# Kernel optimization log

Hardware: AMD Instinct MI355X
Metric: run time of the kernel (lower is better)

The kernel has to match this reference:

```python
import jax, jax.numpy as jnp
import numpy as np

N_PTS = 1 << 20          # query points
N_LEVELS = 8
BASE_RES, MAX_RES = 16, 512
GROWTH = (MAX_RES / BASE_RES) ** (1.0 / (N_LEVELS - 1))
RES = [int(np.floor(BASE_RES * GROWTH ** i)) for i in range(N_LEVELS)]
T = 1 << 19              # hash table size per level
F = 2                    # features per table entry
D = 64                   # per-level MLP width
NUM_OUT = 16
BOUND = 1.5

# 8 corner offsets of a unit cube, and NGP spatial-hash primes
OFFSETS = np.stack(np.meshgrid(*([[0, 1]] * 3), indexing='ij'), -1).reshape(8, 3)
PRIMES = np.array([1, 2654435761, 805459861], dtype=np.uint32)


def hash_interp(xn, table, res):
    """Trilinear hash-grid lookup. xn: [N,3] in [0,1), table: [T,F]."""
    pos = xn * res                                    # [N,3]
    p0f = jnp.floor(pos)
    w = pos - jax.lax.stop_gradient(p0f)              # [N,3] interp weights
    p0 = jax.lax.stop_gradient(p0f).astype(jnp.uint32)
    corners = p0[:, None, :] + jnp.asarray(OFFSETS.astype(np.uint32))[None]  # [N,8,3]
    hp = corners * jnp.asarray(PRIMES)[None, None, :]  # uint32 wraparound mul
    idx = (hp[..., 0] ^ hp[..., 1] ^ hp[..., 2]) & jnp.uint32(T - 1)  # [N,8]
    feats = table[idx]                                # [N,8,F] irregular gather
    off = jnp.asarray(OFFSETS.astype(np.float32))     # [8,3]
    wc = jnp.prod(off[None] * w[:, None, :] + (1.0 - off[None]) * (1.0 - w[:, None, :]), axis=-1)  # [N,8]
    return jnp.einsum('nc,ncf->nf', wc, feats)        # [N,F]


def fourier(h, B):
    """Fourier feature embed: h [N,D] @ B [N_freqs] -> [sin, cos]."""
    proj = (2.0 * jnp.pi) * (h @ B)                   # [N, D//2]
    return jnp.concatenate([jnp.sin(proj), jnp.cos(proj)], axis=-1)  # [N, D]


def setup_inputs() -> dict:
    key = jax.random.key(0)
    ks = jax.random.split(key, 12)
    inp = {
        'input': jax.random.normal(ks[0], (N_PTS, 3), jnp.float32),
        'W0': jax.random.normal(ks[1], (3, D), jnp.float32) * 0.3,
        'b0': jnp.zeros((D,), jnp.float32),
        'Ws': jax.random.normal(ks[2], (N_LEVELS - 1, D, D), jnp.float32) * (1.0 / np.sqrt(D)),
        'bs': jnp.zeros((N_LEVELS - 1, D), jnp.float32),
        'tables': jax.random.uniform(ks[3], (N_LEVELS, T, F), jnp.float32, -1e-2, 1e-2),
        'Gw': jax.random.normal(ks[4], (N_LEVELS, F, D), jnp.float32) * 0.5,
        'Gb': jnp.zeros((N_LEVELS, D), jnp.float32),
        'Bmat': jax.random.normal(ks[5], (N_LEVELS, D, D // 2), jnp.float32) * 0.25,
        'Wout': jax.random.normal(ks[6], (D, NUM_OUT), jnp.float32) * (1.0 / np.sqrt(D)),
        'bout': jnp.zeros((NUM_OUT,), jnp.float32),
    }
    return inp


def reference(input, W0, b0, Ws, bs, tables, Gw, Gb, Bmat, Wout, bout):
    x = input / BOUND                                  # [N,3]
    xn = jnp.clip((x + 1.0) * 0.5, 0.0, 1.0 - 1e-6)    # normalize to [0,1)
    h = x
    acc = jnp.zeros((input.shape[0], D), jnp.float32)
    for i in range(N_LEVELS):
        h = (h @ W0 + b0) if i == 0 else (h @ Ws[i - 1] + bs[i - 1])  # [N,D]
        g = hash_interp(xn, tables[i], float(RES[i]))  # [N,F] hash-grid feats
        hg = h + g @ Gw[i] + Gb[i]                     # fuse grid feats into channel
        acc = acc + fourier(hg, Bmat[i])               # [N,D] sin/cos embed, summed
    return acc @ Wout + bout                           # [N,NUM_OUT]
```

## Files before the change

### kernel.cpp

```cpp
#include <hip/hip_runtime.h>
#include <math.h>
#include <stdint.h>

#define N_LEVELS 8
#define TBITS 19
#define TMASK ((1u << TBITS) - 1u)
#define BLK 128

typedef __attribute__((ext_vector_type(8))) short short8;
typedef __attribute__((ext_vector_type(4))) float f32x4;
typedef unsigned int uint;
typedef unsigned short ushort;

#define WSW_OFF   0
#define WSW_N     (7 * 2 * 4 * 2 * 512)
#define WSB_OFF   (WSW_N * 2)
#define WSB_N     (8 * 2 * 2 * 2 * 512)
#define WSWO_OFF  (WSB_OFF + WSB_N * 2)
#define WSWO_N    (2 * 2 * 512)
#define WSP_OFF   (WSWO_OFF + WSWO_N * 2)
#define WSP_N     (8 * 3 * 32)
#define WS_NEEDED ((size_t)(WSP_OFF + WSP_N * 4))

struct ResArr { float r[N_LEVELS]; };

#define HIDX(pt, ch) ((((pt) << 6) | (ch)) ^ (((pt) & 7) << 3))
#define HLO 2048

__device__ __forceinline__ ushort f2bf(float f) {
    uint u = __float_as_uint(f);
    u += 0x7fffu + ((u >> 16) & 1u);
    return (ushort)(u >> 16);
}
__device__ __forceinline__ float bf2f(ushort h) {
    return __uint_as_float(((uint)h) << 16);
}
__device__ __forceinline__ uint cvtpk(float a, float b) {
    uint r;
    asm("v_cvt_pk_bf16_f32 %0, %1, %2" : "=v"(r) : "v"(a), "v"(b));
    return r;
}
__device__ __forceinline__ short8 ldfragG(const void* p) {
    return __builtin_bit_cast(short8, *(const uint4*)p);
}
__device__ __forceinline__ short8 ldfragL(const ushort* p) {
    return __builtin_bit_cast(short8, *(const uint4*)p);
}
__device__ __forceinline__ f32x4 MFMA(short8 a, short8 b, f32x4 c) {
    return __builtin_amdgcn_mfma_f32_16x16x32_bf16(a, b, c, 0, 0, 0);
}
__device__ __forceinline__ f32x4 zero4() {
    f32x4 z; z[0] = 0.f; z[1] = 0.f; z[2] = 0.f; z[3] = 0.f; return z;
}
__device__ __forceinline__ float sin2pi(float t) {
    return __builtin_amdgcn_sinf(__builtin_amdgcn_fractf(t));
}
__device__ __forceinline__ float cos2pi(float t) {
    return __builtin_amdgcn_cosf(__builtin_amdgcn_fractf(t));
}

__global__ void prep_kernel(const float* __restrict__ Ws,
                            const float* __restrict__ Bmat,
                            const float* __restrict__ Wout,
                            const float* __restrict__ Gw,
                            const float* __restrict__ Gb,
                            void* __restrict__ ws)
{
    const int NW = WSW_N, NB = WSB_N, NWO = WSWO_N;
    const int NTOT = NW + NB + NWO + WSP_N;
    int t = blockIdx.x * 256 + threadIdx.x;
    if (t >= NTOT) return;
    ushort* w16 = (ushort*)ws;
    float* wsP = (float*)((char*)ws + WSP_OFF);

    if (t < NW) {
        int i = t & 7, lane = (t >> 3) & 63, ks = (t >> 9) & 1;
        int mb = (t >> 10) & 3, s = (t >> 12) & 1, lv = t >> 13;
        int gl = lane >> 4, il = lane & 15;
        int k = ks * 32 + gl * 8 + i, m = mb * 16 + il;
        float v = Ws[lv * 4096 + k * 64 + m];
        ushort hi = f2bf(v);
        w16[t] = s ? f2bf(v - bf2f(hi)) : hi;
    } else if (t < NW + NB) {
        int u = t - NW;
        int i = u & 7, lane = (u >> 3) & 63, ks = (u >> 9) & 1;
        int mb = (u >> 10) & 1, s = (u >> 11) & 1, lv = u >> 12;
        int gl = lane >> 4, il = lane & 15;
        int k = ks * 32 + gl * 8 + i, m = mb * 16 + il;
        float v = Bmat[lv * 2048 + k * 32 + m];
        ushort hi = f2bf(v);
        w16[NW + u] = s ? f2bf(v - bf2f(hi)) : hi;
    } else if (t < NW + NB + NWO) {
        int u = t - NW - NB;
        int i = u & 7, lane = (u >> 3) & 63, ks = (u >> 9) & 1, s = (u >> 10) & 1;
        int gl = lane >> 4, il = lane & 15;
        int k = ks * 32 + gl * 8 + i;
        float v = Wout[k * 16 + il];
        ushort hi = f2bf(v);
        w16[(WSWO_OFF / 2) + u] = s ? f2bf(v - bf2f(hi)) : hi;
    } else {
        int u = t - NW - NB - NWO;
        int lv = u / 96, rem = u % 96, wh = rem >> 5, m = rem & 31;
        const float* src = (wh == 0) ? (Gw + lv * 128)
                         : (wh == 1) ? (Gw + lv * 128 + 64)
                                     : (Gb + lv * 64);
        float acc = 0.f;
        for (int j = 0; j < 64; ++j)
            acc = fmaf(src[j], Bmat[lv * 2048 + j * 32 + m], acc);
        wsP[lv * 96 + wh * 32 + m] = acc;
    }
}

__global__ __launch_bounds__(64) void ffb_mfma(
    const float* __restrict__ input,
    const float* __restrict__ W0,
    const float* __restrict__ b0,
    const float* __restrict__ bs,
    const float* __restrict__ tables,
    const float* __restrict__ bout,
    const void* __restrict__ ws,
    float* __restrict__ out,
    int npts, ResArr ra)
{
    __shared__ __attribute__((aligned(16))) ushort sH[4096];
    __shared__ float sP[96];
    __shared__ float sBias[64];
    __shared__ float sG[64];

    const int l = threadIdx.x;
    const int il = l & 15, gl = l >> 4;
    const int base = blockIdx.x * 32;
    const int p = l & 31;
    const char* wsc = (const char*)ws;
    const float* wsP = (const float*)(wsc + WSP_OFF);

    float x0 = input[(size_t)(base + p) * 3 + 0] * (1.0f / 1.5f);
    float x1 = input[(size_t)(base + p) * 3 + 1] * (1.0f / 1.5f);
    float x2 = input[(size_t)(base + p) * 3 + 2] * (1.0f / 1.5f);
    const float hiclip = (float)(1.0 - 1e-6);
    float xn0 = fminf(fmaxf((x0 + 1.0f) * 0.5f, 0.0f), hiclip);
    float xn1 = fminf(fmaxf((x1 + 1.0f) * 0.5f, 0.0f), hiclip);
    float xn2 = fminf(fmaxf((x2 + 1.0f) * 0.5f, 0.0f), hiclip);

    short8 aWo[2];
#pragma unroll
    for (int ks = 0; ks < 2; ++ks)
        aWo[ks] = ldfragG(wsc + WSWO_OFF + (size_t)ks * 1024 + l * 16);

    f32x4 outacc[2];
    outacc[0] = zero4(); outacc[1] = zero4();
    short8 bH0[2][2], bH1[2][2];

    for (int lev = 0; lev < N_LEVELS; ++lev) {
        if (lev > 0) sBias[l] = bs[(lev - 1) * 64 + l];
        sP[l] = wsP[lev * 96 + l];
        if (l < 32) sP[64 + l] = wsP[lev * 96 + 64 + l];
        if (l < 32) {
            const float res = ra.r[lev];
            float px = xn0 * res, py = xn1 * res, pz = xn2 * res;
            float fx = floorf(px), fy = floorf(py), fz = floorf(pz);
            float wx = px - fx, wy = py - fy, wz = pz - fz;
            uint ix = (uint)fx, iy = (uint)fy, iz = (uint)fz;
            const float* __restrict__ tab = tables + (((size_t)lev) << TBITS) * 2;
            float g0 = 0.f, g1 = 0.f;
#pragma unroll
            for (int c = 0; c < 8; ++c) {
                const uint bx = (c >> 2) & 1, by = (c >> 1) & 1, bz = c & 1;
                uint hx = ix + bx;
                uint hy = (iy + by) * 2654435761u;
                uint hz = (iz + bz) * 805459861u;
                uint idx = (hx ^ hy ^ hz) & TMASK;
                float f0 = tab[(size_t)idx * 2 + 0];
                float f1 = tab[(size_t)idx * 2 + 1];
                float wc = (bx ? wx : 1.0f - wx) * (by ? wy : 1.0f - wy) * (bz ? wz : 1.0f - wz);
                g0 = fmaf(wc, f0, g0);
                g1 = fmaf(wc, f1, g1);
            }
            sG[2 * l] = g0; sG[2 * l + 1] = g1;
        }
        __syncthreads();

        if (lev == 0) {
            const int chb = (l >> 5) * 32;
#pragma unroll
            for (int cc = 0; cc < 32; cc += 2) {
                int ch = chb + cc;
                float v0 = fmaf(x0, W0[ch],     fmaf(x1, W0[64 + ch],     fmaf(x2, W0[128 + ch],     b0[ch])));
                float v1 = fmaf(x0, W0[ch + 1], fmaf(x1, W0[64 + ch + 1], fmaf(x2, W0[128 + ch + 1], b0[ch + 1])));
                uint pk = cvtpk(v0, v1);
                float r0 = v0 - __uint_as_float(pk << 16);
                float r1 = v1 - __uint_as_float(pk & 0xffff0000u);
                uint pklo = cvtpk(r0, r1);
                uint idx = HIDX(p, ch);
                *(uint*)&sH[idx] = pk;
                *(uint*)&sH[HLO + idx] = pklo;
            }
        } else {
            f32x4 acc[4][2];
#pragma unroll
            for (int mb = 0; mb < 4; ++mb)
#pragma unroll
                for (int nb = 0; nb < 2; ++nb) acc[mb][nb] = zero4();
#pragma unroll
            for (int mb = 0; mb < 4; ++mb) {
                short8 aHi[2], aLo[2];
#pragma unroll
                for (int ks = 0; ks < 2; ++ks) {
                    aHi[ks] = ldfragG(wsc + WSW_OFF + (size_t)((((lev - 1) * 2 + 0) * 4 + mb) * 2 + ks) * 1024 + l * 16);
                    aLo[ks] = ldfragG(wsc + WSW_OFF + (size_t)((((lev - 1) * 2 + 1) * 4 + mb) * 2 + ks) * 1024 + l * 16);
                }
#pragma unroll
                for (int nb = 0; nb < 2; ++nb)
#pragma unroll
                    for (int ks = 0; ks < 2; ++ks) {
                        acc[mb][nb] = MFMA(aHi[ks], bH0[ks][nb], acc[mb][nb]);
                        acc[mb][nb] = MFMA(aLo[ks], bH0[ks][nb], acc[mb][nb]);
                        acc[mb][nb] = MFMA(aHi[ks], bH1[ks][nb], acc[mb][nb]);
                    }
            }
#pragma unroll
            for (int mb = 0; mb < 4; ++mb)
#pragma unroll
                for (int nb = 0; nb < 2; ++nb) {
                    int pt = nb * 16 + il, ch0 = mb * 16 + gl * 4;
                    float2 ba = *(float2*)&sBias[ch0];
                    float2 bb = *(float2*)&sBias[ch0 + 2];
                    float v0 = acc[mb][nb][0] + ba.x, v1 = acc[mb][nb][1] + ba.y;
                    float v2 = acc[mb][nb][2] + bb.x, v3 = acc[mb][nb][3] + bb.y;
                    uint pkA = cvtpk(v0, v1), pkB = cvtpk(v2, v3);
                    float r0 = v0 - __uint_as_float(pkA << 16);
                    float r1 = v1 - __uint_as_float(pkA & 0xffff0000u);
                    float r2 = v2 - __uint_as_float(pkB << 16);
                    float r3 = v3 - __uint_as_float(pkB & 0xffff0000u);
                    uint pkLA = cvtpk(r0, r1), pkLB = cvtpk(r2, r3);
                    uint idx = HIDX(pt, ch0);
                    *(uint*)&sH[idx] = pkA;        *(uint*)&sH[idx + 2] = pkB;
                    *(uint*)&sH[HLO + idx] = pkLA; *(uint*)&sH[HLO + idx + 2] = pkLB;
                }
        }
        __syncthreads();

#pragma unroll
        for (int ks = 0; ks < 2; ++ks)
#pragma unroll
            for (int nb = 0; nb < 2; ++nb) {
                int pt = nb * 16 + il;
                uint idx = HIDX(pt, ks * 32 + gl * 8);
                bH0[ks][nb] = ldfragL(&sH[idx]);
                bH1[ks][nb] = ldfragL(&sH[HLO + idx]);
            }

        f32x4 pacc[2][2];
#pragma unroll
        for (int mb = 0; mb < 2; ++mb)
#pragma unroll
            for (int nb = 0; nb < 2; ++nb) pacc[mb][nb] = zero4();
#pragma unroll
        for (int mb = 0; mb < 2; ++mb) {
            short8 aBhi[2], aBlo[2];
#pragma unroll
            for (int ks = 0; ks < 2; ++ks) {
                aBhi[ks] = ldfragG(wsc + WSB_OFF + (size_t)(((lev * 2 + 0) * 2 + mb) * 2 + ks) * 1024 + l * 16);
                aBlo[ks] = ldfragG(wsc + WSB_OFF + (size_t)(((lev * 2 + 1) * 2 + mb) * 2 + ks) * 1024 + l * 16);
            }
#pragma unroll
            for (int nb = 0; nb < 2; ++nb)
#pragma unroll
                for (int ks = 0; ks < 2; ++ks) {
                    pacc[mb][nb] = MFMA(aBhi[ks], bH0[ks][nb], pacc[mb][nb]);
                    pacc[mb][nb] = MFMA(aBlo[ks], bH0[ks][nb], pacc[mb][nb]);
                    pacc[mb][nb] = MFMA(aBhi[ks], bH1[ks][nb], pacc[mb][nb]);
                }
        }

#pragma unroll
        for (int mb = 0; mb < 2; ++mb)
#pragma unroll
            for (int nb = 0; nb < 2; ++nb) {
                int pt = nb * 16 + il, m0 = mb * 16 + gl * 4;
                float2 g   = *(float2*)&sG[pt * 2];
                float2 p0a = *(float2*)&sP[m0],      p0b = *(float2*)&sP[m0 + 2];
                float2 p1a = *(float2*)&sP[32 + m0], p1b = *(float2*)&sP[32 + m0 + 2];
                float2 p2a = *(float2*)&sP[64 + m0], p2b = *(float2*)&sP[64 + m0 + 2];
                float t0 = pacc[mb][nb][0] + fmaf(g.x, p0a.x, fmaf(g.y, p1a.x, p2a.x));
                float t1 = pacc[mb][nb][1] + fmaf(g.x, p0a.y, fmaf(g.y, p1a.y, p2a.y));
                float t2 = pacc[mb][nb][2] + fmaf(g.x, p0b.x, fmaf(g.y, p1b.x, p2b.x));
                float t3 = pacc[mb][nb][3] + fmaf(g.x, p0b.y, fmaf(g.y, p1b.y, p2b.y));
                float s0 = sin2pi(t0), s1 = sin2pi(t1), s2 = sin2pi(t2), s3 = sin2pi(t3);
                float c0 = cos2pi(t0), c1 = cos2pi(t1), c2 = cos2pi(t2), c3 = cos2pi(t3);
                uint idxs = HIDX(pt, m0), idxc = HIDX(pt, 32 + m0);
                *(uint*)&sH[HLO + idxs]     = cvtpk(s0, s1);
                *(uint*)&sH[HLO + idxs + 2] = cvtpk(s2, s3);
                *(uint*)&sH[HLO + idxc]     = cvtpk(c0, c1);
                *(uint*)&sH[HLO + idxc + 2] = cvtpk(c2, c3);
            }
        __syncthreads();

#pragma unroll
        for (int nb = 0; nb < 2; ++nb)
#pragma unroll
            for (int ks = 0; ks < 2; ++ks) {
                int pt = nb * 16 + il;
                short8 bF = ldfragL(&sH[HLO + HIDX(pt, ks * 32 + gl * 8)]);
                outacc[nb] = MFMA(aWo[ks], bF, outacc[nb]);
            }
    }

    float4 bo = *(const float4*)&bout[gl * 4];
#pragma unroll
    for (int nb = 0; nb < 2; ++nb) {
        int pt = nb * 16 + il;
        float4 v;
        v.x = outacc[nb][0] + bo.x;
        v.y = outacc[nb][1] + bo.y;
        v.z = outacc[nb][2] + bo.z;
        v.w = outacc[nb][3] + bo.w;
        *(float4*)(&out[(size_t)(base + pt) * 16 + gl * 4]) = v;
    }
}

__global__ __launch_bounds__(BLK) void ffb_valu(
    const float* __restrict__ input,
    const float* __restrict__ W0,
    const float* __restrict__ b0,
    const float* __restrict__ Ws,
    const float* __restrict__ bs,
    const float* __restrict__ tables,
    const float* __restrict__ Gw,
    const float* __restrict__ Gb,
    const float* __restrict__ Bmat,
    const float* __restrict__ Wout,
    const float* __restrict__ bout,
    float* __restrict__ out,
    int npts, ResArr resarr)
{
    __shared__ float lds_h[64][BLK];

    const int tid = threadIdx.x;
    const int n = blockIdx.x * BLK + tid;
    if (n >= npts) return;

    float x0 = input[(size_t)n * 3 + 0] / 1.5f;
    float x1 = input[(size_t)n * 3 + 1] / 1.5f;
    float x2 = input[(size_t)n * 3 + 2] / 1.5f;
    const float hi = (float)(1.0 - 1e-6);
    float xn0 = fminf(fmaxf((x0 + 1.0f) * 0.5f, 0.0f), hi);
    float xn1 = fminf(fmaxf((x1 + 1.0f) * 0.5f, 0.0f), hi);
    float xn2 = fminf(fmaxf((x2 + 1.0f) * 0.5f, 0.0f), hi);

    float outacc[16];
#pragma unroll
    for (int o = 0; o < 16; ++o) outacc[o] = 0.0f;

    for (int lev = 0; lev < N_LEVELS; ++lev) {
        float nh[64];
        if (lev == 0) {
#pragma unroll
            for (int j = 0; j < 64; ++j)
                nh[j] = fmaf(x0, W0[j], fmaf(x1, W0[64 + j], fmaf(x2, W0[128 + j], b0[j])));
        } else {
            const float* __restrict__ Wl = Ws + (size_t)(lev - 1) * 4096;
            const float* __restrict__ bl = bs + (size_t)(lev - 1) * 64;
#pragma unroll
            for (int j = 0; j < 64; ++j) nh[j] = bl[j];
            for (int k = 0; k < 64; ++k) {
                float hk = lds_h[k][tid];
                const float* __restrict__ wrow = Wl + (size_t)k * 64;
#pragma unroll
                for (int j = 0; j < 64; ++j)
                    nh[j] = fmaf(hk, wrow[j], nh[j]);
            }
        }
#pragma unroll
        for (int j = 0; j < 64; ++j) lds_h[j][tid] = nh[j];

        const float res = resarr.r[lev];
        float px = xn0 * res, py = xn1 * res, pz = xn2 * res;
        float fx = floorf(px), fy = floorf(py), fz = floorf(pz);
        float wx = px - fx, wy = py - fy, wz = pz - fz;
        uint32_t ix = (uint32_t)fx, iy = (uint32_t)fy, iz = (uint32_t)fz;
        const float* __restrict__ tab = tables + ((size_t)lev << TBITS) * 2;
        float g0 = 0.0f, g1 = 0.0f;
#pragma unroll
        for (int c = 0; c < 8; ++c) {
            const uint32_t bx = (c >> 2) & 1, by = (c >> 1) & 1, bz = c & 1;
            uint32_t hx = (ix + bx);
            uint32_t hy = (iy + by) * 2654435761u;
            uint32_t hz = (iz + bz) * 805459861u;
            uint32_t idx = (hx ^ hy ^ hz) & TMASK;
            float f0 = tab[(size_t)idx * 2 + 0];
            float f1 = tab[(size_t)idx * 2 + 1];
            float wc = (bx ? wx : 1.0f - wx) * (by ? wy : 1.0f - wy) * (bz ? wz : 1.0f - wz);
            g0 = fmaf(wc, f0, g0);
            g1 = fmaf(wc, f1, g1);
        }

        const float* __restrict__ Gw0 = Gw + (size_t)lev * 128;
        const float* __restrict__ Gw1 = Gw0 + 64;
        const float* __restrict__ Gbl = Gb + (size_t)lev * 64;
        const float* __restrict__ Bl  = Bmat + (size_t)lev * 2048;
        float proj[32];
#pragma unroll
        for (int m = 0; m < 32; ++m) proj[m] = 0.0f;
        for (int j = 0; j < 64; ++j) {
            float hgj = lds_h[j][tid] + fmaf(g0, Gw0[j], fmaf(g1, Gw1[j], Gbl[j]));
            const float* __restrict__ brow = Bl + (size_t)j * 32;
#pragma unroll
            for (int m = 0; m < 32; ++m)
                proj[m] = fmaf(hgj, brow[m], proj[m]);
        }

#pragma unroll
        for (int m = 0; m < 32; ++m) {
            float s = sin2pi(proj[m]);
            float c = cos2pi(proj[m]);
            const float* __restrict__ wsrow = Wout + (size_t)m * 16;
            const float* __restrict__ wcrow = Wout + (size_t)(m + 32) * 16;
#pragma unroll
            for (int o = 0; o < 16; ++o)
                outacc[o] = fmaf(s, wsrow[o], fmaf(c, wcrow[o], outacc[o]));
        }
    }

#pragma unroll
    for (int o = 0; o < 16; ++o)
        out[(size_t)n * 16 + o] = outacc[o] + bout[o];
}

extern "C" void kernel_launch(void* const* d_in, const int* in_sizes, int n_in,
                              void* d_out, int out_size, void* d_ws, size_t ws_size,
                              hipStream_t stream) {
    const float* input  = (const float*)d_in[0];
    const float* W0     = (const float*)d_in[1];
    const float* b0     = (const float*)d_in[2];
    const float* Ws     = (const float*)d_in[3];
    const float* bs     = (const float*)d_in[4];
    const float* tables = (const float*)d_in[5];
    const float* Gw     = (const float*)d_in[6];
    const float* Gb     = (const float*)d_in[7];
    const float* Bmat   = (const float*)d_in[8];
    const float* Wout   = (const float*)d_in[9];
    const float* bout   = (const float*)d_in[10];
    float* out = (float*)d_out;

    const int npts = in_sizes[0] / 3;

    ResArr ra;
    const double growth = pow(512.0 / 16.0, 1.0 / (double)(N_LEVELS - 1));
    for (int i = 0; i < N_LEVELS; ++i)
        ra.r[i] = (float)floor(16.0 * pow(growth, (double)i));

    if (ws_size >= WS_NEEDED && (npts % 32) == 0) {
        const int NTOT = WSW_N + WSB_N + WSWO_N + WSP_N;
        hipLaunchKernelGGL(prep_kernel, dim3((NTOT + 255) / 256), dim3(256), 0, stream,
                           Ws, Bmat, Wout, Gw, Gb, d_ws);
        hipLaunchKernelGGL(ffb_mfma, dim3(npts / 32), dim3(64), 0, stream,
                           input, W0, b0, bs, tables, bout, d_ws, out, npts, ra);
    } else {
        hipLaunchKernelGGL(ffb_valu, dim3((npts + BLK - 1) / BLK), dim3(BLK), 0, stream,
                           input, W0, b0, Ws, bs, tables, Gw, Gb, Bmat, Wout, bout,
                           out, npts, ra);
    }
}
```

Measured before the change: 754.1 us.

## Halve points per block and spread hash-grid corner gathers across all lanes

Each 64-lane block now handles 16 points instead of 32. Each group of 16 lanes computes two of the eight trilinear corners, and the partial sums are reduced with cross-lane shuffles. This replaces the half-idle hash gather and the LDS round trip through sG. Bias and projection constants are now read directly from global memory instead of staged in LDS, which removes shared buffers and one barrier per level. The cost is twice as many blocks, so weight fragments are reloaded twice as often per point, and each MFMA fragment load is reused over half as many points.

```diff
diff --git a/kernel.cpp b/kernel.cpp
--- a/kernel.cpp
+++ b/kernel.cpp
@@ -25,7 +25,7 @@
 struct ResArr { float r[N_LEVELS]; };
 
 #define HIDX(pt, ch) ((((pt) << 6) | (ch)) ^ (((pt) & 7) << 3))
-#define HLO 2048
+#define HLO 1024
 
 __device__ __forceinline__ ushort f2bf(float f) {
     uint u = __float_as_uint(f);
@@ -122,21 +122,17 @@
     float* __restrict__ out,
     int npts, ResArr ra)
 {
-    __shared__ __attribute__((aligned(16))) ushort sH[4096];
-    __shared__ float sP[96];
-    __shared__ float sBias[64];
-    __shared__ float sG[64];
+    __shared__ __attribute__((aligned(16))) ushort sH[2048];
 
     const int l = threadIdx.x;
     const int il = l & 15, gl = l >> 4;
-    const int base = blockIdx.x * 32;
-    const int p = l & 31;
+    const int base = blockIdx.x * 16;
     const char* wsc = (const char*)ws;
     const float* wsP = (const float*)(wsc + WSP_OFF);
 
-    float x0 = input[(size_t)(base + p) * 3 + 0] * (1.0f / 1.5f);
-    float x1 = input[(size_t)(base + p) * 3 + 1] * (1.0f / 1.5f);
-    float x2 = input[(size_t)(base + p) * 3 + 2] * (1.0f / 1.5f);
+    float x0 = input[(size_t)(base + il) * 3 + 0] * (1.0f / 1.5f);
+    float x1 = input[(size_t)(base + il) * 3 + 1] * (1.0f / 1.5f);
+    float x2 = input[(size_t)(base + il) * 3 + 2] * (1.0f / 1.5f);
     const float hiclip = (float)(1.0 - 1e-6);
     float xn0 = fminf(fmaxf((x0 + 1.0f) * 0.5f, 0.0f), hiclip);
     float xn1 = fminf(fmaxf((x1 + 1.0f) * 0.5f, 0.0f), hiclip);
@@ -147,24 +143,21 @@
     for (int ks = 0; ks < 2; ++ks)
         aWo[ks] = ldfragG(wsc + WSWO_OFF + (size_t)ks * 1024 + l * 16);
 
-    f32x4 outacc[2];
-    outacc[0] = zero4(); outacc[1] = zero4();
-    short8 bH0[2][2], bH1[2][2];
+    f32x4 outacc = zero4();
+    short8 bH0[2], bH1[2];
 
     for (int lev = 0; lev < N_LEVELS; ++lev) {
-        if (lev > 0) sBias[l] = bs[(lev - 1) * 64 + l];
-        sP[l] = wsP[lev * 96 + l];
-        if (l < 32) sP[64 + l] = wsP[lev * 96 + 64 + l];
-        if (l < 32) {
+        float g0 = 0.f, g1 = 0.f;
+        {
             const float res = ra.r[lev];
             float px = xn0 * res, py = xn1 * res, pz = xn2 * res;
             float fx = floorf(px), fy = floorf(py), fz = floorf(pz);
             float wx = px - fx, wy = py - fy, wz = pz - fz;
             uint ix = (uint)fx, iy = (uint)fy, iz = (uint)fz;
             const float* __restrict__ tab = tables + (((size_t)lev) << TBITS) * 2;
-            float g0 = 0.f, g1 = 0.f;
-#pragma unroll
-            for (int c = 0; c < 8; ++c) {
+#pragma unroll
+            for (int j = 0; j < 2; ++j) {
+                const uint c = (uint)(gl * 2 + j);
                 const uint bx = (c >> 2) & 1, by = (c >> 1) & 1, bz = c & 1;
                 uint hx = ix + bx;
                 uint hy = (iy + by) * 2654435761u;
@@ -176,14 +169,14 @@
                 g0 = fmaf(wc, f0, g0);
                 g1 = fmaf(wc, f1, g1);
             }
-            sG[2 * l] = g0; sG[2 * l + 1] = g1;
-        }
-        __syncthreads();
+            g0 += __shfl_xor(g0, 16); g1 += __shfl_xor(g1, 16);
+            g0 += __shfl_xor(g0, 32); g1 += __shfl_xor(g1, 32);
+        }
 
         if (lev == 0) {
-            const int chb = (l >> 5) * 32;
-#pragma unroll
-            for (int cc = 0; cc < 32; cc += 2) {
+            const int chb = gl * 16;
+#pragma unroll
+            for (int cc = 0; cc < 16; cc += 2) {
                 int ch = chb + cc;
                 float v0 = fmaf(x0, W0[ch],     fmaf(x1, W0[64 + ch],     fmaf(x2, W0[128 + ch],     b0[ch])));
                 float v1 = fmaf(x0, W0[ch + 1], fmaf(x1, W0[64 + ch + 1], fmaf(x2, W0[128 + ch + 1], b0[ch + 1])));
@@ -191,16 +184,14 @@
                 float r0 = v0 - __uint_as_float(pk << 16);
                 float r1 = v1 - __uint_as_float(pk & 0xffff0000u);
                 uint pklo = cvtpk(r0, r1);
-                uint idx = HIDX(p, ch);
+                uint idx = HIDX(il, ch);
                 *(uint*)&sH[idx] = pk;
                 *(uint*)&sH[HLO + idx] = pklo;
             }
         } else {
-            f32x4 acc[4][2];
-#pragma unroll
-            for (int mb = 0; mb < 4; ++mb)
-#pragma unroll
-                for (int nb = 0; nb < 2; ++nb) acc[mb][nb] = zero4();
+            f32x4 acc[4];
+#pragma unroll
+            for (int mb = 0; mb < 4; ++mb) acc[mb] = zero4();
 #pragma unroll
             for (int mb = 0; mb < 4; ++mb) {
                 short8 aHi[2], aLo[2];
@@ -210,51 +201,40 @@
                     aLo[ks] = ldfragG(wsc + WSW_OFF + (size_t)((((lev - 1) * 2 + 1) * 4 + mb) * 2 + ks) * 1024 + l * 16);
                 }
 #pragma unroll
-                for (int nb = 0; nb < 2; ++nb)
-#pragma unroll
-                    for (int ks = 0; ks < 2; ++ks) {
-                        acc[mb][nb] = MFMA(aHi[ks], bH0[ks][nb], acc[mb][nb]);
-                        acc[mb][nb] = MFMA(aLo[ks], bH0[ks][nb], acc[mb][nb]);
-                        acc[mb][nb] = MFMA(aHi[ks], bH1[ks][nb], acc[mb][nb]);
-                    }
-            }
-#pragma unroll
-            for (int mb = 0; mb < 4; ++mb)
-#pragma unroll
-                for (int nb = 0; nb < 2; ++nb) {
-                    int pt = nb * 16 + il, ch0 = mb * 16 + gl * 4;
-                    float2 ba = *(float2*)&sBias[ch0];
-                    float2 bb = *(float2*)&sBias[ch0 + 2];
-                    float v0 = acc[mb][nb][0] + ba.x, v1 = acc[mb][nb][1] + ba.y;
-                    float v2 = acc[mb][nb][2] + bb.x, v3 = acc[mb][nb][3] + bb.y;
-                    uint pkA = cvtpk(v0, v1), pkB = cvtpk(v2, v3);
-                    float r0 = v0 - __uint_as_float(pkA << 16);
-                    float r1 = v1 - __uint_as_float(pkA & 0xffff0000u);
-                    float r2 = v2 - __uint_as_float(pkB << 16);
-                    float r3 = v3 - __uint_as_float(pkB & 0xffff0000u);
-                    uint pkLA = cvtpk(r0, r1), pkLB = cvtpk(r2, r3);
-                    uint idx = HIDX(pt, ch0);
-                    *(uint*)&sH[idx] = pkA;        *(uint*)&sH[idx + 2] = pkB;
-                    *(uint*)&sH[HLO + idx] = pkLA; *(uint*)&sH[HLO + idx + 2] = pkLB;
+                for (int ks = 0; ks < 2; ++ks) {
+                    acc[mb] = MFMA(aHi[ks], bH0[ks], acc[mb]);
+                    acc[mb] = MFMA(aLo[ks], bH0[ks], acc[mb]);
+                    acc[mb] = MFMA(aHi[ks], bH1[ks], acc[mb]);
                 }
+            }
+#pragma unroll
+            for (int mb = 0; mb < 4; ++mb) {
+                int ch0 = mb * 16 + gl * 4;
+                float4 bb = *(const float4*)&bs[(size_t)(lev - 1) * 64 + ch0];
+                float v0 = acc[mb][0] + bb.x, v1 = acc[mb][1] + bb.y;
+                float v2 = acc[mb][2] + bb.z, v3 = acc[mb][3] + bb.w;
+                uint pkA = cvtpk(v0, v1), pkB = cvtpk(v2, v3);
+                float r0 = v0 - __uint_as_float(pkA << 16);
+                float r1 = v1 - __uint_as_float(pkA & 0xffff0000u);
+                float r2 = v2 - __uint_as_float(pkB << 16);
+                float r3 = v3 - __uint_as_float(pkB & 0xffff0000u);
+                uint pkLA = cvtpk(r0, r1), pkLB = cvtpk(r2, r3);
+                uint idx = HIDX(il, ch0);
+                *(uint*)&sH[idx] = pkA;        *(uint*)&sH[idx + 2] = pkB;
+                *(uint*)&sH[HLO + idx] = pkLA; *(uint*)&sH[HLO + idx + 2] = pkLB;
+            }
         }
         __syncthreads();
 
 #pragma unroll
-        for (int ks = 0; ks < 2; ++ks)
-#pragma unroll
-            for (int nb = 0; nb < 2; ++nb) {
-                int pt = nb * 16 + il;
-                uint idx = HIDX(pt, ks * 32 + gl * 8);
-                bH0[ks][nb] = ldfragL(&sH[idx]);
-                bH1[ks][nb] = ldfragL(&sH[HLO + idx]);
-            }
-
-        f32x4 pacc[2][2];
-#pragma unroll
-        for (int mb = 0; mb < 2; ++mb)
-#pragma unroll
-            for (int nb = 0; nb < 2; ++nb) pacc[mb][nb] = zero4();
+        for (int ks = 0; ks < 2; ++ks) {
+            uint idx = HIDX(il, ks * 32 + gl * 8);
+            bH0[ks] = ldfragL(&sH[idx]);
+            bH1[ks] = ldfragL(&sH[HLO + idx]);
+        }
+
+        f32x4 pacc[2];
+        pacc[0] = zero4(); pacc[1] = zero4();
 #pragma unroll
         for (int mb = 0; mb < 2; ++mb) {
             short8 aBhi[2], aBlo[2];
@@ -264,59 +244,48 @@
                 aBlo[ks] = ldfragG(wsc + WSB_OFF + (size_t)(((lev * 2 + 1) * 2 + mb) * 2 + ks) * 1024 + l * 16);
             }
 #pragma unroll
-            for (int nb = 0; nb < 2; ++nb)
-#pragma unroll
-                for (int ks = 0; ks < 2; ++ks) {
-                    pacc[mb][nb] = MFMA(aBhi[ks], bH0[ks][nb], pacc[mb][nb]);
-                    pacc[mb][nb] = MFMA(aBlo[ks], bH0[ks][nb], pacc[mb][nb]);
-                    pacc[mb][nb] = MFMA(aBhi[ks], bH1[ks][nb], pacc[mb][nb]);
-                }
-        }
-
-#pragma unroll
-        for (int mb = 0; mb < 2; ++mb)
-#pragma unroll
-            for (int nb = 0; nb < 2; ++nb) {
-                int pt = nb * 16 + il, m0 = mb * 16 + gl * 4;
-                float2 g   = *(float2*)&sG[pt * 2];
-                float2 p0a = *(float2*)&sP[m0],      p0b = *(float2*)&sP[m0 + 2];
-                float2 p1a = *(float2*)&sP[32 + m0], p1b = *(float2*)&sP[32 + m0 + 2];
-                float2 p2a = *(float2*)&sP[64 + m0], p2b = *(float2*)&sP[64 + m0 + 2];
-                float t0 = pacc[mb][nb][0] + fmaf(g.x, p0a.x, fmaf(g.y, p1a.x, p2a.x));
-                float t1 = pacc[mb][nb][1] + fmaf(g.x, p0a.y, fmaf(g.y, p1a.y, p2a.y));
-                float t2 = pacc[mb][nb][2] + fmaf(g.x, p0b.x, fmaf(g.y, p1b.x, p2b.x));
-                float t3 = pacc[mb][nb][3] + fmaf(g.x, p0b.y, fmaf(g.y, p1b.y, p2b.y));
-                float s0 = sin2pi(t0), s1 = sin2pi(t1), s2 = sin2pi(t2), s3 = sin2pi(t3);
-                float c0 = cos2pi(t0), c1 = cos2pi(t1), c2 = cos2pi(t2), c3 = cos2pi(t3);
-                uint idxs = HIDX(pt, m0), idxc = HIDX(pt, 32 + m0);
-                *(uint*)&sH[HLO + idxs]     = cvtpk(s0, s1);
-                *(uint*)&sH[HLO + idxs + 2] = cvtpk(s2, s3);
-                *(uint*)&sH[HLO + idxc]     = cvtpk(c0, c1);
-                *(uint*)&sH[HLO + idxc + 2] = cvtpk(c2, c3);
-            }
+            for (int ks = 0; ks < 2; ++ks) {
+                pacc[mb] = MFMA(aBhi[ks], bH0[ks], pacc[mb]);
+                pacc[mb] = MFMA(aBlo[ks], bH0[ks], pacc[mb]);
+                pacc[mb] = MFMA(aBhi[ks], bH1[ks], pacc[mb]);
+            }
+        }
+
+#pragma unroll
+        for (int mb = 0; mb < 2; ++mb) {
+            int m0 = mb * 16 + gl * 4;
+            const float* __restrict__ Pb = wsP + lev * 96;
+            float4 P0 = *(const float4*)&Pb[m0];
+            float4 P1 = *(const float4*)&Pb[32 + m0];
+            float4 P2 = *(const float4*)&Pb[64 + m0];
+            float t0 = pacc[mb][0] + fmaf(g0, P0.x, fmaf(g1, P1.x, P2.x));
+            float t1 = pacc[mb][1] + fmaf(g0, P0.y, fmaf(g1, P1.y, P2.y));
+            float t2 = pacc[mb][2] + fmaf(g0, P0.z, fmaf(g1, P1.z, P2.z));
+            float t3 = pacc[mb][3] + fmaf(g0, P0.w, fmaf(g1, P1.w, P2.w));
+            float s0 = sin2pi(t0), s1 = sin2pi(t1), s2 = sin2pi(t2), s3 = sin2pi(t3);
+            float c0 = cos2pi(t0), c1 = cos2pi(t1), c2 = cos2pi(t2), c3 = cos2pi(t3);
+            uint idxs = HIDX(il, m0), idxc = HIDX(il, 32 + m0);
+            *(uint*)&sH[HLO + idxs]     = cvtpk(s0, s1);
+            *(uint*)&sH[HLO + idxs + 2] = cvtpk(s2, s3);
+            *(uint*)&sH[HLO + idxc]     = cvtpk(c0, c1);
+            *(uint*)&sH[HLO + idxc + 2] = cvtpk(c2, c3);
+        }
         __syncthreads();
 
 #pragma unroll
-        for (int nb = 0; nb < 2; ++nb)
-#pragma unroll
-            for (int ks = 0; ks < 2; ++ks) {
-                int pt = nb * 16 + il;
-                short8 bF = ldfragL(&sH[HLO + HIDX(pt, ks * 32 + gl * 8)]);
-                outacc[nb] = MFMA(aWo[ks], bF, outacc[nb]);
-            }
+        for (int ks = 0; ks < 2; ++ks) {
+            short8 bF = ldfragL(&sH[HLO + HIDX(il, ks * 32 + gl * 8)]);
+            outacc = MFMA(aWo[ks], bF, outacc);
+        }
     }
 
     float4 bo = *(const float4*)&bout[gl * 4];
-#pragma unroll
-    for (int nb = 0; nb < 2; ++nb) {
-        int pt = nb * 16 + il;
-        float4 v;
-        v.x = outacc[nb][0] + bo.x;
-        v.y = outacc[nb][1] + bo.y;
-        v.z = outacc[nb][2] + bo.z;
-        v.w = outacc[nb][3] + bo.w;
-        *(float4*)(&out[(size_t)(base + pt) * 16 + gl * 4]) = v;
-    }
+    float4 v;
+    v.x = outacc[0] + bo.x;
+    v.y = outacc[1] + bo.y;
+    v.z = outacc[2] + bo.z;
+    v.w = outacc[3] + bo.w;
+    *(float4*)(&out[(size_t)(base + il) * 16 + gl * 4]) = v;
 }
 
 __global__ __launch_bounds__(BLK) void ffb_valu(
@@ -450,11 +419,11 @@
     for (int i = 0; i < N_LEVELS; ++i)
         ra.r[i] = (float)floor(16.0 * pow(growth, (double)i));
 
-    if (ws_size >= WS_NEEDED && (npts % 32) == 0) {
+    if (ws_size >= WS_NEEDED && (npts % 16) == 0) {
         const int NTOT = WSW_N + WSB_N + WSWO_N + WSP_N;
         hipLaunchKernelGGL(prep_kernel, dim3((NTOT + 255) / 256), dim3(256), 0, stream,
                            Ws, Bmat, Wout, Gw, Gb, d_ws);
-        hipLaunchKernelGGL(ffb_mfma, dim3(npts / 32), dim3(64), 0, stream,
+        hipLaunchKernelGGL(ffb_mfma, dim3(npts / 16), dim3(64), 0, stream,
                            input, W0, b0, bs, tables, bout, d_ws, out, npts, ra);
     } else {
         hipLaunchKernelGGL(ffb_valu, dim3((npts + BLK - 1) / BLK), dim3(BLK), 0, stream,
```

Result: faster. 697.4 us (-7.5%).
